# Kernel optimization log

Measured on AMD Instinct MI355X. Metric: run time of the kernel, lower is better.

The kernel has to match this reference:

```python
import jax, jax.numpy as jnp
import numpy as np

B, H, N, D = 8, 12, 1024, 64
SCALE = 1.0 / float(np.sqrt(D))  # 0.125; torch forward default is 1.0 but 1/sqrt(d) is the production value
EPS = 1e-06


def setup_inputs() -> dict:
    key = jax.random.key(0)
    kq, kk, kv = jax.random.split(key, 3)
    q = jax.random.normal(kq, (B, H, N, D), dtype=jnp.float32)
    k = jax.random.normal(kk, (B, H, N, D), dtype=jnp.float32)
    v = jax.random.normal(kv, (B, H, N, D), dtype=jnp.float32)
    # Parameter init per L2Q.__init__: alpha=0.125, beta=0.5, gamma=1/n_tokens
    alpha = jnp.full((H, 1, 1), 0.125, dtype=jnp.float32)
    beta = jnp.full((H, 1, 1), 0.5, dtype=jnp.float32)
    gamma = jnp.full((H, 1, 1), 1.0 / N, dtype=jnp.float32)
    return {"q": q, "k": k, "v": v, "alpha": alpha, "beta": beta, "gamma": gamma}


def reference(q, k, v, alpha, beta, gamma):
    # logits: (B, H, N, N)
    logits = jnp.einsum("bhnd,bhmd->bhnm", q, k) * SCALE
    # per-head quadratic polynomial, then ReLU; params (H,1,1) broadcast over (B,H,N,N)
    attn = jax.nn.relu(alpha * logits * logits + beta * logits + gamma)
    attn = attn / (jnp.sum(attn, axis=-1, keepdims=True) + EPS)
    return jnp.einsum("bhnm,bhmd->bhnd", attn, v)
```

## Files before the change

kernel.cpp:

```cpp
#include <hip/hip_runtime.h>
#include <hip/hip_bf16.h>

typedef __attribute__((ext_vector_type(8))) short bf16x8;
typedef __attribute__((ext_vector_type(4))) float f32x4;

#define MFMA16(a, b, c) __builtin_amdgcn_mfma_f32_16x16x32_bf16(a, b, c, 0, 0, 0)

static constexpr int kH = 12;
static constexpr int kN = 1024;
static constexpr int kD = 64;
static constexpr int kTiles = kN / 64;
static constexpr float kScale = 0.125f;
static constexpr float kEps = 1e-6f;

static constexpr int KSU = 36;
static constexpr int VSU = 36;
static constexpr int PSU = 36;

__device__ __forceinline__ unsigned bfbits(float x) {
    union { __hip_bfloat16 h; unsigned short u; } c;
    c.h = __float2bfloat16(x);
    return (unsigned)c.u;
}
__device__ __forceinline__ unsigned pack2(float a, float b) {
    return bfbits(a) | (bfbits(b) << 16);
}

__global__ __launch_bounds__(256, 3) void l2q_attn(
    const float* __restrict__ q, const float* __restrict__ k, const float* __restrict__ v,
    const float* __restrict__ alpha, const float* __restrict__ beta, const float* __restrict__ gamma,
    float* __restrict__ out)
{
    __shared__ __align__(16) unsigned KsU[64 * KSU];
    __shared__ __align__(16) unsigned VtU[64 * VSU];
    __shared__ __align__(16) unsigned PU[128 * PSU];

    const int bid  = blockIdx.x;
    const int bh   = bid >> 3;
    const int qt   = bid & 7;
    const int h    = bh % kH;
    const int t    = threadIdx.x;
    const int wave = t >> 6;
    const int lane = t & 63;
    const int quad = lane >> 4;
    const int l15  = lane & 15;

    const float al = alpha[h], be = beta[h], ga = gamma[h];

    const long base = (long)bh * kN * kD;
    const float* qp = q + base;
    const float* kp = k + base;
    const float* vp = v + base;

    bf16x8 qa[2][2];
#pragma unroll
    for (int rb = 0; rb < 2; ++rb) {
        const int row = qt * 128 + wave * 32 + rb * 16 + l15;
#pragma unroll
        for (int kc = 0; kc < 2; ++kc) {
            const float* src = qp + (long)row * kD + kc * 32 + quad * 8;
            const float4 f0 = *(const float4*)(src);
            const float4 f1 = *(const float4*)(src + 4);
            bf16x8 a;
            a[0] = (short)bfbits(f0.x); a[1] = (short)bfbits(f0.y);
            a[2] = (short)bfbits(f0.z); a[3] = (short)bfbits(f0.w);
            a[4] = (short)bfbits(f1.x); a[5] = (short)bfbits(f1.y);
            a[6] = (short)bfbits(f1.z); a[7] = (short)bfbits(f1.w);
            qa[rb][kc] = a;
        }
    }

    f32x4 oacc[2][4];
#pragma unroll
    for (int rb = 0; rb < 2; ++rb)
#pragma unroll
        for (int db = 0; db < 4; ++db)
            oacc[rb][db] = (f32x4){0.f, 0.f, 0.f, 0.f};

    float dsum[2][4] = {{0.f, 0.f, 0.f, 0.f}, {0.f, 0.f, 0.f, 0.f}};

    unsigned* Pw = &PU[wave * 32 * PSU];

    for (int tile = 0; tile < kTiles; ++tile) {
        __syncthreads();
        const int k0 = tile * 64;

#pragma unroll
        for (int r = 0; r < 4; ++r) {
            const int f4 = t + 256 * r;
            const int n = f4 >> 4, d4 = f4 & 15;
            const float4 kg = *(const float4*)(kp + (long)(k0 + n) * kD + 4 * d4);
            uint2 pk;
            pk.x = pack2(kg.x, kg.y);
            pk.y = pack2(kg.z, kg.w);
            *(uint2*)&KsU[n * KSU + 2 * d4] = pk;
        }
#pragma unroll
        for (int r = 0; r < 2; ++r) {
            const int u = t + 256 * r;
            const int key2 = u & 31, d4 = u >> 5;
            const float* s0 = vp + (long)(k0 + 2 * key2) * kD + 4 * d4;
            const float4 va = *(const float4*)(s0);
            const float4 vb = *(const float4*)(s0 + kD);
            VtU[(4 * d4 + 0) * VSU + key2] = pack2(va.x, vb.x);
            VtU[(4 * d4 + 1) * VSU + key2] = pack2(va.y, vb.y);
            VtU[(4 * d4 + 2) * VSU + key2] = pack2(va.z, vb.z);
            VtU[(4 * d4 + 3) * VSU + key2] = pack2(va.w, vb.w);
        }
        __syncthreads();

        f32x4 s[2][4];
#pragma unroll
        for (int rb = 0; rb < 2; ++rb)
#pragma unroll
            for (int nb = 0; nb < 4; ++nb)
                s[rb][nb] = (f32x4){0.f, 0.f, 0.f, 0.f};
#pragma unroll
        for (int nb = 0; nb < 4; ++nb) {
            bf16x8 kb0 = *(const bf16x8*)&KsU[(nb * 16 + l15) * KSU + 4 * quad];
            bf16x8 kb1 = *(const bf16x8*)&KsU[(nb * 16 + l15) * KSU + 16 + 4 * quad];
#pragma unroll
            for (int rb = 0; rb < 2; ++rb) {
                s[rb][nb] = MFMA16(qa[rb][0], kb0, s[rb][nb]);
                s[rb][nb] = MFMA16(qa[rb][1], kb1, s[rb][nb]);
            }
        }

        const bool ev = (lane & 1) == 0;
#pragma unroll
        for (int rb = 0; rb < 2; ++rb) {
#pragma unroll
            for (int nb = 0; nb < 4; ++nb) {
                float w0, w1, w2, w3;
                {
                    float l0 = s[rb][nb][0] * kScale;
                    float l1 = s[rb][nb][1] * kScale;
                    float l2 = s[rb][nb][2] * kScale;
                    float l3 = s[rb][nb][3] * kScale;
                    w0 = fmaxf(fmaf(fmaf(al, l0, be), l0, ga), 0.f);
                    w1 = fmaxf(fmaf(fmaf(al, l1, be), l1, ga), 0.f);
                    w2 = fmaxf(fmaf(fmaf(al, l2, be), l2, ga), 0.f);
                    w3 = fmaxf(fmaf(fmaf(al, l3, be), l3, ga), 0.f);
                }
                dsum[rb][0] += w0; dsum[rb][1] += w1;
                dsum[rb][2] += w2; dsum[rb][3] += w3;

                const float o0 = __shfl_xor(w0, 1);
                const float o1 = __shfl_xor(w1, 1);
                const float o2 = __shfl_xor(w2, 1);
                const float o3 = __shfl_xor(w3, 1);
                const unsigned pa = ev ? pack2(w0, o0) : pack2(o2, w2);
                const unsigned pb = ev ? pack2(w1, o1) : pack2(o3, w3);
                const int r0 = ev ? 0 : 2;
                const int cu = (16 * nb + (l15 & ~1)) >> 1;
                const int rowb = rb * 16 + quad * 4 + r0;
                Pw[rowb * PSU + cu] = pa;
                Pw[(rowb + 1) * PSU + cu] = pb;
            }
        }

        bf16x8 pf[2][2];
#pragma unroll
        for (int rb = 0; rb < 2; ++rb)
#pragma unroll
            for (int kc = 0; kc < 2; ++kc)
                pf[rb][kc] = *(const bf16x8*)&Pw[(rb * 16 + l15) * PSU + 16 * kc + 4 * quad];
#pragma unroll
        for (int db = 0; db < 4; ++db) {
            bf16x8 vf0 = *(const bf16x8*)&VtU[(db * 16 + l15) * VSU + 4 * quad];
            bf16x8 vf1 = *(const bf16x8*)&VtU[(db * 16 + l15) * VSU + 16 + 4 * quad];
#pragma unroll
            for (int rb = 0; rb < 2; ++rb) {
                oacc[rb][db] = MFMA16(pf[rb][0], vf0, oacc[rb][db]);
                oacc[rb][db] = MFMA16(pf[rb][1], vf1, oacc[rb][db]);
            }
        }
    }

#pragma unroll
    for (int rb = 0; rb < 2; ++rb)
#pragma unroll
        for (int i = 0; i < 4; ++i) {
            float d = dsum[rb][i];
            d += __shfl_xor(d, 1);
            d += __shfl_xor(d, 2);
            d += __shfl_xor(d, 4);
            d += __shfl_xor(d, 8);
            dsum[rb][i] = 1.0f / (d + kEps);
        }

#pragma unroll
    for (int rb = 0; rb < 2; ++rb)
#pragma unroll
        for (int db = 0; db < 4; ++db)
#pragma unroll
            for (int i = 0; i < 4; ++i) {
                const int row = qt * 128 + wave * 32 + rb * 16 + quad * 4 + i;
                out[base + (long)row * kD + db * 16 + l15] = oacc[rb][db][i] * dsum[rb][i];
            }
}

extern "C" void kernel_launch(void* const* d_in, const int* in_sizes, int n_in,
                              void* d_out, int out_size, void* d_ws, size_t ws_size,
                              hipStream_t stream) {
    const float* q     = (const float*)d_in[0];
    const float* k     = (const float*)d_in[1];
    const float* v     = (const float*)d_in[2];
    const float* alpha = (const float*)d_in[3];
    const float* beta  = (const float*)d_in[4];
    const float* gamma = (const float*)d_in[5];
    float* out = (float*)d_out;

    l2q_attn<<<dim3(768), dim3(256), 0, stream>>>(q, k, v, alpha, beta, gamma, out);
}
```

Before: 162.6 us.

## Pre-cast Q/K/V to bf16 in workspace and double-buffer K/V via direct LDS loads

Adds two pre-pass kernels that convert Q and K to bf16 and write a transposed bf16 V into the workspace. The main kernel then streams K/V tiles with global_load_lds into double-buffered, XOR-swizzled shared memory, so the next tile's load overlaps compute. Other changes: the scale is folded into the polynomial coefficients, P is packed with a cheaper round-half-up conversion, and S is computed transposed so row sums need fewer shuffles. In exchange it adds two extra launches and a round trip of the inputs through global memory. It falls back to the old kernel when the workspace is too small.

```diff
diff --git a/kernel.cpp b/kernel.cpp
--- a/kernel.cpp
+++ b/kernel.cpp
@@ -9,24 +9,242 @@
 static constexpr int kH = 12;
 static constexpr int kN = 1024;
 static constexpr int kD = 64;
+static constexpr int kBH = 96;
+static constexpr int kND = kN * kD;
 static constexpr int kTiles = kN / 64;
 static constexpr float kScale = 0.125f;
 static constexpr float kEps = 1e-6f;
-
-static constexpr int KSU = 36;
-static constexpr int VSU = 36;
-static constexpr int PSU = 36;
+static constexpr long kTensorElems = (long)kBH * kND;
+static constexpr long kWsNeeded = 3 * kTensorElems * 2;
 
 __device__ __forceinline__ unsigned bfbits(float x) {
     union { __hip_bfloat16 h; unsigned short u; } c;
     c.h = __float2bfloat16(x);
     return (unsigned)c.u;
 }
-__device__ __forceinline__ unsigned pack2(float a, float b) {
+__device__ __forceinline__ unsigned pack2_rne(float a, float b) {
     return bfbits(a) | (bfbits(b) << 16);
 }
-
-__global__ __launch_bounds__(256, 3) void l2q_attn(
+__device__ __forceinline__ unsigned pack2_rhu(float lo, float hi) {
+    unsigned a = __builtin_bit_cast(unsigned, lo) + 0x8000u;
+    unsigned b = __builtin_bit_cast(unsigned, hi) + 0x8000u;
+    return __builtin_amdgcn_perm(b, a, 0x07060302u);
+}
+
+__device__ __forceinline__ void gl_lds16(const void* g, void* l) {
+    __builtin_amdgcn_global_load_lds(
+        (const __attribute__((address_space(1))) void*)g,
+        (__attribute__((address_space(3))) void*)l, 16, 0, 0);
+}
+
+__global__ __launch_bounds__(256, 4) void cast_qk(
+    const float* __restrict__ q, const float* __restrict__ k,
+    unsigned* __restrict__ qo, unsigned* __restrict__ ko)
+{
+    const int tid = blockIdx.x * 256 + threadIdx.x;
+    const int stride = 1536 * 256;
+    const long perT = kTensorElems / 4;
+#pragma unroll
+    for (int r = 0; r < 8; ++r) {
+        long i = (long)tid + (long)r * stride;
+        const float4* src; unsigned* dst; long j;
+        if (i < perT) { src = (const float4*)q; dst = qo; j = i; }
+        else          { src = (const float4*)k; dst = ko; j = i - perT; }
+        float4 f = src[j];
+        uint2 u;
+        u.x = pack2_rne(f.x, f.y);
+        u.y = pack2_rne(f.z, f.w);
+        *(uint2*)&dst[j * 2] = u;
+    }
+}
+
+__global__ __launch_bounds__(256, 4) void vtrans(
+    const float* __restrict__ v, unsigned* __restrict__ vt)
+{
+    static constexpr int TS = 68;
+    __shared__ float T32[64 * TS];
+    const int bid = blockIdx.x;
+    const int bh = bid >> 4, kt = bid & 15;
+    const int t = threadIdx.x;
+    const float* vp = v + (long)bh * kND + (long)kt * 64 * kD;
+
+#pragma unroll
+    for (int r = 0; r < 4; ++r) {
+        const int f4 = t + 256 * r;
+        const int n = f4 >> 4, d4 = f4 & 15;
+        const float4 f = *(const float4*)(vp + (long)n * kD + 4 * d4);
+        *(float4*)&T32[n * TS + 4 * d4] = f;
+    }
+    __syncthreads();
+
+    const int d = t >> 2, c = t & 3;
+    unsigned u[8];
+#pragma unroll
+    for (int j = 0; j < 8; ++j) {
+        const int key = c * 16 + 2 * j;
+        u[j] = pack2_rne(T32[key * TS + d], T32[(key + 1) * TS + d]);
+    }
+    unsigned* dst = vt + (long)bh * (kND / 2) + (long)d * (kN / 2) + kt * 32 + c * 8;
+    *(uint4*)(dst)     = *(uint4*)&u[0];
+    *(uint4*)(dst + 4) = *(uint4*)&u[4];
+}
+
+__global__ __launch_bounds__(256, 3) void l2q_main(
+    const unsigned short* __restrict__ qbf, const unsigned short* __restrict__ kbf,
+    const unsigned short* __restrict__ vtbf,
+    const float* __restrict__ alpha, const float* __restrict__ beta, const float* __restrict__ gamma,
+    float* __restrict__ out)
+{
+    __shared__ __align__(16) unsigned Ks[2][2048];
+    __shared__ __align__(16) unsigned Vs[2][2048];
+    __shared__ __align__(16) unsigned Pu[4][1024];
+
+    const int bid  = blockIdx.x;
+    const int bh   = bid >> 3;
+    const int qt   = bid & 7;
+    const int h    = bh % kH;
+    const int t    = threadIdx.x;
+    const int wave = t >> 6;
+    const int lane = t & 63;
+    const int quad = lane >> 4;
+    const int l15  = lane & 15;
+    const int sw   = l15 & 7;
+
+    const float al = alpha[h] * (kScale * kScale);
+    const float be = beta[h] * kScale;
+    const float ga = gamma[h];
+
+    const unsigned short* qp = qbf + (long)bh * kND;
+    const unsigned short* kp = kbf + (long)bh * kND;
+    const unsigned short* vp = vtbf + (long)bh * kND;
+
+    bf16x8 qa[2][2];
+#pragma unroll
+    for (int qb = 0; qb < 2; ++qb) {
+        const int row = qt * 128 + wave * 32 + qb * 16 + l15;
+#pragma unroll
+        for (int kc = 0; kc < 2; ++kc)
+            qa[qb][kc] = *(const bf16x8*)(qp + (long)row * kD + kc * 32 + quad * 8);
+    }
+
+    f32x4 oacc[2][4];
+#pragma unroll
+    for (int qb = 0; qb < 2; ++qb)
+#pragma unroll
+        for (int db = 0; db < 4; ++db)
+            oacc[qb][db] = (f32x4){0.f, 0.f, 0.f, 0.f};
+    f32x4 dsv[2] = {(f32x4){0.f,0.f,0.f,0.f}, (f32x4){0.f,0.f,0.f,0.f}};
+
+    const int srow = lane >> 3;
+    const int g    = lane & 7;
+    auto stageKV = [&](int buf, int tile) {
+        const int k0 = tile * 64;
+#pragma unroll
+        for (int c = 0; c < 2; ++c) {
+            const int r  = (c * 4 + wave) * 8 + srow;
+            const int gl = (g ^ (r & 7)) * 8;
+            gl_lds16(kp + (long)(k0 + r) * kD + gl, &Ks[buf][(c * 4 + wave) * 256]);
+            gl_lds16(vp + (long)r * kN + k0 + gl,   &Vs[buf][(c * 4 + wave) * 256]);
+        }
+    };
+
+    stageKV(0, 0);
+
+    unsigned* Pw = Pu[wave];
+
+    for (int tile = 0; tile < kTiles; ++tile) {
+        const int buf = tile & 1;
+        __syncthreads();
+        if (tile + 1 < kTiles) stageKV(buf ^ 1, tile + 1);
+
+        const unsigned* Kb = Ks[buf];
+        const unsigned* Vb = Vs[buf];
+
+        f32x4 st[2][4];
+#pragma unroll
+        for (int qb = 0; qb < 2; ++qb)
+#pragma unroll
+            for (int kb = 0; kb < 4; ++kb)
+                st[qb][kb] = (f32x4){0.f, 0.f, 0.f, 0.f};
+#pragma unroll
+        for (int kb = 0; kb < 4; ++kb) {
+            const int row = kb * 16 + l15;
+            bf16x8 kf0 = *(const bf16x8*)&Kb[row * 32 + ((quad ^ sw) << 2)];
+            bf16x8 kf1 = *(const bf16x8*)&Kb[row * 32 + (((4 + quad) ^ sw) << 2)];
+#pragma unroll
+            for (int qb = 0; qb < 2; ++qb) {
+                st[qb][kb] = MFMA16(kf0, qa[qb][0], st[qb][kb]);
+                st[qb][kb] = MFMA16(kf1, qa[qb][1], st[qb][kb]);
+            }
+        }
+
+#pragma unroll
+        for (int qb = 0; qb < 2; ++qb) {
+            const int pbase = (qb * 16 + l15) * 32;
+#pragma unroll
+            for (int kb = 0; kb < 4; ++kb) {
+                f32x4 s = st[qb][kb];
+                f32x4 w = s * al + be;
+                w = w * s + ga;
+                w[0] = fmaxf(w[0], 0.f); w[1] = fmaxf(w[1], 0.f);
+                w[2] = fmaxf(w[2], 0.f); w[3] = fmaxf(w[3], 0.f);
+                dsv[qb] += w;
+                uint2 pk2;
+                pk2.x = pack2_rhu(w[0], w[1]);
+                pk2.y = pack2_rhu(w[2], w[3]);
+                const int col = kb * 8 + quad * 2;
+                const int gr = col >> 2, off = col & 3;
+                *(uint2*)&Pw[pbase + ((gr ^ sw) << 2) + off] = pk2;
+            }
+        }
+
+        bf16x8 pf[2][2];
+#pragma unroll
+        for (int qb = 0; qb < 2; ++qb) {
+            const int pbase = (qb * 16 + l15) * 32;
+            pf[qb][0] = *(const bf16x8*)&Pw[pbase + ((quad ^ sw) << 2)];
+            pf[qb][1] = *(const bf16x8*)&Pw[pbase + (((4 + quad) ^ sw) << 2)];
+        }
+#pragma unroll
+        for (int db = 0; db < 4; ++db) {
+            const int vrow = db * 16 + l15;
+            bf16x8 vf0 = *(const bf16x8*)&Vb[vrow * 32 + ((quad ^ sw) << 2)];
+            bf16x8 vf1 = *(const bf16x8*)&Vb[vrow * 32 + (((4 + quad) ^ sw) << 2)];
+#pragma unroll
+            for (int qb = 0; qb < 2; ++qb) {
+                oacc[qb][db] = MFMA16(pf[qb][0], vf0, oacc[qb][db]);
+                oacc[qb][db] = MFMA16(pf[qb][1], vf1, oacc[qb][db]);
+            }
+        }
+    }
+
+    float dr[2];
+#pragma unroll
+    for (int qb = 0; qb < 2; ++qb) {
+        float d = dsv[qb][0] + dsv[qb][1] + dsv[qb][2] + dsv[qb][3];
+        d += __shfl_xor(d, 16);
+        d += __shfl_xor(d, 32);
+        dr[qb] = 1.0f / (d + kEps);
+    }
+
+    const long obase = (long)bh * kND;
+#pragma unroll
+    for (int qb = 0; qb < 2; ++qb)
+#pragma unroll
+        for (int i = 0; i < 4; ++i) {
+            const float rr = __shfl(dr[qb], quad * 4 + i);
+            const int row = qt * 128 + wave * 32 + qb * 16 + quad * 4 + i;
+#pragma unroll
+            for (int db = 0; db < 4; ++db)
+                out[obase + (long)row * kD + db * 16 + l15] = oacc[qb][db][i] * rr;
+        }
+}
+
+static constexpr int KSU = 36;
+static constexpr int VSU = 36;
+static constexpr int PSU = 36;
+
+__global__ __launch_bounds__(256, 3) void l2q_attn_fb(
     const float* __restrict__ q, const float* __restrict__ k, const float* __restrict__ v,
     const float* __restrict__ alpha, const float* __restrict__ beta, const float* __restrict__ gamma,
     float* __restrict__ out)
@@ -78,21 +296,19 @@
             oacc[rb][db] = (f32x4){0.f, 0.f, 0.f, 0.f};
 
     float dsum[2][4] = {{0.f, 0.f, 0.f, 0.f}, {0.f, 0.f, 0.f, 0.f}};
-
     unsigned* Pw = &PU[wave * 32 * PSU];
 
     for (int tile = 0; tile < kTiles; ++tile) {
         __syncthreads();
         const int k0 = tile * 64;
-
 #pragma unroll
         for (int r = 0; r < 4; ++r) {
             const int f4 = t + 256 * r;
             const int n = f4 >> 4, d4 = f4 & 15;
             const float4 kg = *(const float4*)(kp + (long)(k0 + n) * kD + 4 * d4);
             uint2 pk;
-            pk.x = pack2(kg.x, kg.y);
-            pk.y = pack2(kg.z, kg.w);
+            pk.x = pack2_rne(kg.x, kg.y);
+            pk.y = pack2_rne(kg.z, kg.w);
             *(uint2*)&KsU[n * KSU + 2 * d4] = pk;
         }
 #pragma unroll
@@ -102,10 +318,10 @@
             const float* s0 = vp + (long)(k0 + 2 * key2) * kD + 4 * d4;
             const float4 va = *(const float4*)(s0);
             const float4 vb = *(const float4*)(s0 + kD);
-            VtU[(4 * d4 + 0) * VSU + key2] = pack2(va.x, vb.x);
-            VtU[(4 * d4 + 1) * VSU + key2] = pack2(va.y, vb.y);
-            VtU[(4 * d4 + 2) * VSU + key2] = pack2(va.z, vb.z);
-            VtU[(4 * d4 + 3) * VSU + key2] = pack2(va.w, vb.w);
+            VtU[(4 * d4 + 0) * VSU + key2] = pack2_rne(va.x, vb.x);
+            VtU[(4 * d4 + 1) * VSU + key2] = pack2_rne(va.y, vb.y);
+            VtU[(4 * d4 + 2) * VSU + key2] = pack2_rne(va.z, vb.z);
+            VtU[(4 * d4 + 3) * VSU + key2] = pack2_rne(va.w, vb.w);
         }
         __syncthreads();
 
@@ -149,8 +365,8 @@
                 const float o1 = __shfl_xor(w1, 1);
                 const float o2 = __shfl_xor(w2, 1);
                 const float o3 = __shfl_xor(w3, 1);
-                const unsigned pa = ev ? pack2(w0, o0) : pack2(o2, w2);
-                const unsigned pb = ev ? pack2(w1, o1) : pack2(o3, w3);
+                const unsigned pa = ev ? pack2_rne(w0, o0) : pack2_rne(o2, w2);
+                const unsigned pb = ev ? pack2_rne(w1, o1) : pack2_rne(o3, w3);
                 const int r0 = ev ? 0 : 2;
                 const int cu = (16 * nb + (l15 & ~1)) >> 1;
                 const int rowb = rb * 16 + quad * 4 + r0;
@@ -211,5 +427,18 @@
     const float* gamma = (const float*)d_in[5];
     float* out = (float*)d_out;
 
-    l2q_attn<<<dim3(768), dim3(256), 0, stream>>>(q, k, v, alpha, beta, gamma, out);
-}
+    if (ws_size < (size_t)kWsNeeded) {
+        l2q_attn_fb<<<dim3(768), dim3(256), 0, stream>>>(q, k, v, alpha, beta, gamma, out);
+        return;
+    }
+
+    unsigned* qbf = (unsigned*)d_ws;
+    unsigned* kbf = qbf + kTensorElems / 2;
+    unsigned* vtb = kbf + kTensorElems / 2;
+
+    cast_qk<<<dim3(1536), dim3(256), 0, stream>>>(q, k, qbf, kbf);
+    vtrans<<<dim3(1536), dim3(256), 0, stream>>>(v, vtb);
+    l2q_main<<<dim3(768), dim3(256), 0, stream>>>(
+        (const unsigned short*)qbf, (const unsigned short*)kbf, (const unsigned short*)vtb,
+        alpha, beta, gamma, out);
+}
```

Result: faster. 158.5 us (-2.6%).
